# Kernel optimization log

Measured on AMD Instinct MI355X. Metric: run time of the kernel, lower is better.

Reference implementation:

```python
import jax, jax.numpy as jnp
import numpy as np

B, T, I, H, O = 64, 512, 256, 1024, 256


def setup_inputs() -> dict:
    key = jax.random.key(0)
    ks = jax.random.split(key, 12)
    s_i = 1.0 / np.sqrt(H)
    u = lambda k, shape: jax.random.uniform(k, shape, jnp.float32, -s_i, s_i)
    return {
        "x": jax.random.normal(ks[0], (B, T, I), jnp.float32),
        "enc_Wih": u(ks[1], (4 * H, I)),
        "enc_Whh": u(ks[2], (4 * H, H)),
        "enc_bih": u(ks[3], (4 * H,)),
        "enc_bhh": u(ks[4], (4 * H,)),
        "dec_Wih": u(ks[5], (4 * H, I)),
        "dec_Whh": u(ks[6], (4 * H, H)),
        "dec_bih": u(ks[7], (4 * H,)),
        "dec_bhh": u(ks[8], (4 * H,)),
        "fc_W": u(ks[9], (O, H)),
        "fc_b": u(ks[10], (O,)),
    }


def _lstm_gates(pre):
    # torch gate order: i, f, g, o
    i, f, g, o = jnp.split(pre, 4, axis=-1)
    return jax.nn.sigmoid(i), jax.nn.sigmoid(f), jnp.tanh(g), jax.nn.sigmoid(o)


def reference(x, enc_Wih, enc_Whh, enc_bih, enc_bhh,
              dec_Wih, dec_Whh, dec_bih, dec_bhh, fc_W, fc_b):
    # ---- encoder: LSTM scan over time, zero initial state ----
    b = enc_bih + enc_bhh  # [4H]
    # precompute input projections for all steps: [T, B, 4H]
    x_t = jnp.swapaxes(x, 0, 1)  # [T, B, I]
    xproj = jnp.einsum('tbi,gi->tbg', x_t, enc_Wih) + b

    def cell(carry, xp):
        h, c = carry
        pre = xp + h @ enc_Whh.T  # [B, 4H]
        i, f, g, o = _lstm_gates(pre)
        c = f * c + i * g
        h = o * jnp.tanh(c)
        return (h, c), None

    h0 = jnp.zeros((B, H), x.dtype)
    c0 = jnp.zeros((B, H), x.dtype)
    (h, c), _ = jax.lax.scan(cell, (h0, c0), xproj)

    # ---- decoder: each frame is ONE LSTM cell step from the SAME (h, c),
    # since the torch loop re-passes encoder state every iteration -> batch over T.
    pre = (jnp.einsum('bti,gi->btg', x, dec_Wih)
           + (h @ dec_Whh.T + dec_bih + dec_bhh)[:, None, :])  # [B, T, 4H]
    i, f, g, o = _lstm_gates(pre)
    c_new = f * c[:, None, :] + i * g          # [B, T, H]
    h_new = o * jnp.tanh(c_new)                # [B, T, H]
    pred = jnp.einsum('bth,oh->bto', h_new, fc_W) + fc_b  # [B, T, O]
    return pred
```

## Files before the change

### kernel.cpp

```cpp
#include <hip/hip_runtime.h>
#include <hip/hip_bf16.h>

#define BB 64
#define TT_ 512
#define IN_ 256
#define HH 1024
#define G4 4096
#define OO 256

typedef _Float16 half8 __attribute__((ext_vector_type(8)));
typedef float f32x4 __attribute__((ext_vector_type(4)));
typedef unsigned int uint4v __attribute__((ext_vector_type(4)));

__device__ __forceinline__ float sigmoidf_(float v) {
    return 1.f / (1.f + __expf(-v));
}
__device__ __forceinline__ float tanhf_(float v) {
    float vc = fminf(fmaxf(v, -15.f), 15.f);
    float e = __expf(2.f * vc);
    return (e - 1.f) / (e + 1.f);
}

__global__ __launch_bounds__(256)
void pack_a2(const float* __restrict__ Whh, const float* __restrict__ Wih,
             _Float16* __restrict__ Apk)
{
    int id = blockIdx.x * 256 + threadIdx.x;
    int dq  = id / 5120;
    int r1  = id - dq * 5120;
    int t2  = r1 / 2560;
    int r2  = r1 - t2 * 2560;
    int kc  = r2 >> 6, l = r2 & 63;
    int rD  = l & 15;
    int g   = rD & 3, ddl = rD >> 2;
    int d   = dq * 8 + t2 * 4 + ddl;
    int j   = g * HH + d;
    int k0  = kc * 32 + ((l >> 4) << 3);
    half8 v;
    if (kc < 32) {
        const float* s = Whh + (size_t)j * HH + k0;
#pragma unroll
        for (int e = 0; e < 8; ++e) v[e] = (_Float16)s[e];
    } else {
        const float* s = Wih + (size_t)j * IN_ + (k0 - 1024);
#pragma unroll
        for (int e = 0; e < 8; ++e) v[e] = (_Float16)s[e];
    }
    ((half8*)Apk)[id] = v;
}

__global__ __launch_bounds__(256)
void pack_ahh(const float* __restrict__ Whh, _Float16* __restrict__ Ahhpk)
{
    int id = blockIdx.x * 256 + threadIdx.x;
    int jt = id >> 11;
    int r  = id & 2047;
    int kc = r >> 6, l = r & 63;
    int rD = l & 15, g = rD & 3, ddl = rD >> 2;
    int d  = jt * 4 + ddl;
    int j  = g * HH + d;
    int k0 = kc * 32 + ((l >> 4) << 3);
    const float* s = Whh + (size_t)j * HH + k0;
    half8 v;
#pragma unroll
    for (int e = 0; e < 8; ++e) v[e] = (_Float16)s[e];
    ((half8*)Ahhpk)[id] = v;
}

__global__ __launch_bounds__(256)
void pack_adec(const float* __restrict__ Wih, _Float16* __restrict__ Adecpk)
{
    int id = blockIdx.x * 256 + threadIdx.x;
    int dq = id >> 10;
    int r1 = id & 1023;
    int t2 = r1 >> 9;
    int r2 = r1 & 511;
    int kc2 = r2 >> 6, l = r2 & 63;
    int rD = l & 15, g = rD & 3, ddl = rD >> 2;
    int d  = dq * 8 + t2 * 4 + ddl;
    int j  = g * HH + d;
    int k0 = kc2 * 32 + ((l >> 4) << 3);
    const float* s = Wih + (size_t)j * IN_ + k0;
    half8 v;
#pragma unroll
    for (int e = 0; e < 8; ++e) v[e] = (_Float16)s[e];
    ((half8*)Adecpk)[id] = v;
}

__global__ __launch_bounds__(256)
void pack_fcw(const float* __restrict__ fcW, _Float16* __restrict__ fcWpk)
{
    int id = blockIdx.x * 256 + threadIdx.x;
    int ot = id >> 11;
    int r  = id & 2047;
    int kc = r >> 6, l = r & 63;
    int o  = ot * 16 + (l & 15);
    int k0 = kc * 32 + ((l >> 4) << 3);
    const float* s = fcW + (size_t)o * HH + k0;
    half8 v;
#pragma unroll
    for (int e = 0; e < 8; ++e) v[e] = (_Float16)s[e];
    ((half8*)fcWpk)[id] = v;
}

__global__ __launch_bounds__(256)
void pack_x(const float* __restrict__ x, _Float16* __restrict__ Xpk)
{
    int id = blockIdx.x * 256 + threadIdx.x;
    int l = id & 63, bt = (id >> 6) & 3, kc2 = (id >> 8) & 7, t = id >> 11;
    int b  = bt * 16 + (l & 15);
    int i0 = kc2 * 32 + ((l >> 4) << 3);
    const float* s = x + ((size_t)b * TT_ + t) * IN_ + i0;
    half8 v;
#pragma unroll
    for (int e = 0; e < 8; ++e) v[e] = (_Float16)s[e];
    ((half8*)Xpk)[id] = v;
}

__global__ __launch_bounds__(256)
void pack_bias(const float* __restrict__ bih, const float* __restrict__ bhh,
               float* __restrict__ biasc)
{
    int j = blockIdx.x * 256 + threadIdx.x;
    if (j < G4) biasc[j] = bih[j] + bhh[j];
}

__global__ __launch_bounds__(256, 1)
void enc_persist(const _Float16* __restrict__ Apk,
                 const _Float16* __restrict__ Xpk,
                 _Float16* __restrict__ Hbuf,
                 const float* __restrict__ biasc,
                 float* __restrict__ cT)
{
    __shared__ __align__(16) _Float16 Ald[4 * 32 * 64 * 8];
    __shared__ __align__(16) f32x4 pp[16 * 64];
    const int tid  = threadIdx.x;
    const int lane = tid & 63, w = tid >> 6;
    const int dq16 = blockIdx.x >> 2, grp = blockIdx.x & 3;
    const int q = lane >> 4, bl = lane & 15;
    const int d = dq16 * 16 + w * 4 + q;
    const int b = grp * 16 + bl;

    {
        const half8* src = (const half8*)Apk + ((size_t)(dq16 * 4 + w) * 40) * 64 + lane;
        half8* dst = (half8*)Ald + (size_t)w * 2048 + lane;
#pragma unroll
        for (int kc = 0; kc < 32; ++kc) dst[kc * 64] = src[kc * 64];
    }
    half8 xa[8];
    {
        const half8* src = (const half8*)Apk + ((size_t)(dq16 * 4 + w) * 40 + 32) * 64 + lane;
#pragma unroll
        for (int k = 0; k < 8; ++k) xa[k] = src[k * 64];
    }

    float bsum[4];
#pragma unroll
    for (int g = 0; g < 4; ++g) bsum[g] = biasc[g * HH + d];

    const half8* Ald8 = (const half8*)Ald + lane;

    const unsigned int pidx = ((unsigned)grp * 2048 + ((unsigned)d >> 5) * 64 +
                               (((unsigned)d >> 3) & 3) * 16 + bl) * 8 + (d & 7);

    float c_reg = 0.f;
    __syncthreads();

    for (int t = 0; t < TT_; ++t) {
        const int sIn  = (t - 1) & 63;
        const int sOut = t & 63;
        const int sPoi = (t + 8) & 63;

        const uint4v* Xsrc = (const uint4v*)Xpk + ((size_t)t * 32 + grp) * 64 + lane;
        uint4v xft[8];
#pragma unroll
        for (int k = 0; k < 8; ++k) {
            asm volatile("global_load_dwordx4 %0, %1, off"
                         : "=v"(xft[k]) : "v"(Xsrc + k * 256));
        }
        uint4v tmp[8];
        const uint4v* Hsrc = (const uint4v*)Hbuf + (size_t)sIn * 8192 +
                             (size_t)grp * 2048;
        if (t > 0) {
#pragma unroll
            for (int i = 0; i < 8; ++i) {
                asm volatile("global_load_dwordx4 %0, %1, off sc0 sc1"
                             : "=v"(tmp[i]) : "v"(Hsrc + i * 256 + tid));
            }
            asm volatile("s_waitcnt vmcnt(8)" ::: "memory");
        } else {
            asm volatile("s_waitcnt vmcnt(0)" ::: "memory");
        }
        __builtin_amdgcn_sched_barrier(0);

        f32x4 accX = {0.f, 0.f, 0.f, 0.f};
#pragma unroll
        for (int k = 0; k < 8; ++k) {
            half8 bf = __builtin_bit_cast(half8, xft[k]);
            accX = __builtin_amdgcn_mfma_f32_16x16x32_f16(xa[k], bf, accX, 0, 0, 0);
        }

        f32x4 accT[4];
#pragma unroll
        for (int jl = 0; jl < 4; ++jl) accT[jl] = (f32x4){0.f, 0.f, 0.f, 0.f};

        if (t > 0) {
            for (;;) {
                asm volatile("s_waitcnt vmcnt(0)" ::: "memory");
                __builtin_amdgcn_sched_barrier(0);
                int bad[8];
                int any = 0;
#pragma unroll
                for (int i = 0; i < 8; ++i) {
                    bad[i] = (tmp[i].x == 0xFFFFFFFFu) | (tmp[i].y == 0xFFFFFFFFu) |
                             (tmp[i].z == 0xFFFFFFFFu) | (tmp[i].w == 0xFFFFFFFFu);
                    any |= bad[i];
                }
                if (__all(any == 0)) break;
#pragma unroll
                for (int i = 0; i < 8; ++i) {
                    if (bad[i]) {
                        asm volatile("global_load_dwordx4 %0, %1, off sc0 sc1"
                                     : "=v"(tmp[i]) : "v"(Hsrc + i * 256 + tid));
                    }
                }
                __builtin_amdgcn_s_sleep(1);
            }

#pragma unroll
            for (int i = 0; i < 8; ++i) {
                const int kc = i * 4 + w;
                half8 bf = __builtin_bit_cast(half8, tmp[i]);
#pragma unroll
                for (int jl = 0; jl < 4; ++jl) {
                    half8 a = Ald8[jl * 2048 + kc * 64];
                    accT[jl] = __builtin_amdgcn_mfma_f32_16x16x32_f16(a, bf, accT[jl], 0, 0, 0);
                }
            }
        }

#pragma unroll
        for (int jl = 0; jl < 4; ++jl)
            pp[(w * 4 + jl) * 64 + lane] = accT[jl];
        __syncthreads();

        f32x4 s = accX;
#pragma unroll
        for (int w2 = 0; w2 < 4; ++w2)
            s += pp[(w2 * 4 + w) * 64 + lane];

        float pi = s[0] + bsum[0];
        float pf = s[1] + bsum[1];
        float pg = s[2] + bsum[2];
        float po = s[3] + bsum[3];
        float ig = sigmoidf_(pi), fg = sigmoidf_(pf);
        float gg = tanhf_(pg),    og = sigmoidf_(po);
        c_reg = fg * c_reg + ig * gg;
        float h = og * tanhf_(c_reg);

        float hp = __shfl_xor(h, 16);
        if (!(q & 1)) {
            _Float16 h0 = (_Float16)h, h1 = (_Float16)hp;
            unsigned int pk = (unsigned int)__builtin_bit_cast(unsigned short, h0) |
                              ((unsigned int)__builtin_bit_cast(unsigned short, h1) << 16);
            unsigned int* po_ = (unsigned int*)(Hbuf + (size_t)sOut * 65536 + pidx);
            asm volatile("global_store_dword %0, %1, off sc0 sc1"
                         :: "v"(po_), "v"(pk) : "memory");
            unsigned int* pz = (unsigned int*)(Hbuf + (size_t)sPoi * 65536 + pidx);
            unsigned int poison = 0xFFFFFFFFu;
            asm volatile("global_store_dword %0, %1, off sc0 sc1"
                         :: "v"(pz), "v"(poison) : "memory");
        }

        if (t < TT_ - 1) __syncthreads();
    }

    cT[d * 64 + b] = c_reg;
}

__global__ __launch_bounds__(256)
void hdec_mfma(const _Float16* __restrict__ Ahhpk,
               const _Float16* __restrict__ Hfin,
               const float* __restrict__ biascd,
               float* __restrict__ hdecg)
{
    const int tid = threadIdx.x;
    const int lane = tid & 63, w = tid >> 6;
    const int jt = blockIdx.x * 4 + w;
    const int q = lane >> 4, bl = lane & 15;

    const half8* A8 = (const half8*)Ahhpk + ((size_t)jt * 32) * 64 + lane;
    const half8* H8 = (const half8*)Hfin + lane;

    f32x4 acc[4];
#pragma unroll
    for (int g = 0; g < 4; ++g) acc[g] = (f32x4){0.f, 0.f, 0.f, 0.f};
#pragma unroll 4
    for (int kc = 0; kc < 32; ++kc) {
        half8 a = A8[kc * 64];
#pragma unroll
        for (int g = 0; g < 4; ++g) {
            half8 bf = H8[g * 2048 + kc * 64];
            acc[g] = __builtin_amdgcn_mfma_f32_16x16x32_f16(a, bf, acc[g], 0, 0, 0);
        }
    }
    int d = jt * 4 + q;
#pragma unroll
    for (int g = 0; g < 4; ++g)
#pragma unroll
        for (int r = 0; r < 4; ++r)
            hdecg[((size_t)r * HH + d) * 64 + g * 16 + bl] = acc[g][r] + biascd[r * HH + d];
}

__global__ __launch_bounds__(256)
void dec_mfma(const _Float16* __restrict__ Adecpk,
              const _Float16* __restrict__ fcWpk,
              const _Float16* __restrict__ Xpk,
              const float* __restrict__ hdecg,
              const float* __restrict__ cT,
              const float* __restrict__ fcb,
              float* __restrict__ out)
{
    __shared__ __align__(16) _Float16 Hn[32 * 64 * 8];
    __shared__ __align__(16) float outl[16][260];
    const int tid = threadIdx.x;
    const int lane = tid & 63, w = tid >> 6;
    const int t = blockIdx.x >> 2, bq4 = blockIdx.x & 3;
    const int q = lane >> 4, bl = lane & 15;
    const int bg = bq4 * 16 + bl;

    const half8* X8 = (const half8*)Xpk + ((size_t)t * 32 + bq4) * 64 + lane;
    half8 xf[8];
#pragma unroll
    for (int kc2 = 0; kc2 < 8; ++kc2) xf[kc2] = X8[kc2 * 256];

    const half8* AD = (const half8*)Adecpk + lane;
    for (int dqi = 0; dqi < 32; ++dqi) {
        int dq = w * 32 + dqi;
#pragma unroll
        for (int t2 = 0; t2 < 2; ++t2) {
            f32x4 acc = {0.f, 0.f, 0.f, 0.f};
#pragma unroll
            for (int kc2 = 0; kc2 < 8; ++kc2) {
                half8 a = AD[((size_t)(dq * 2 + t2) * 8 + kc2) * 64];
                acc = __builtin_amdgcn_mfma_f32_16x16x32_f16(a, xf[kc2], acc, 0, 0, 0);
            }
            int d = dq * 8 + t2 * 4 + q;
            float cv = cT[d * 64 + bg];
            float pi = acc[0] + hdecg[(size_t)(0 * HH + d) * 64 + bg];
            float pf = acc[1] + hdecg[(size_t)(1 * HH + d) * 64 + bg];
            float pg = acc[2] + hdecg[(size_t)(2 * HH + d) * 64 + bg];
            float po = acc[3] + hdecg[(size_t)(3 * HH + d) * 64 + bg];
            float ig = sigmoidf_(pi), fg = sigmoidf_(pf);
            float gg = tanhf_(pg),    og = sigmoidf_(po);
            float cn = fg * cv + ig * gg;
            float h = og * tanhf_(cn);
            Hn[((d >> 5) * 64 + ((d >> 3) & 3) * 16 + bl) * 8 + (d & 7)] = (_Float16)h;
        }
    }
    __syncthreads();

    const half8* Hn8 = (const half8*)Hn + lane;
    const half8* FW = (const half8*)fcWpk + lane;
#pragma unroll
    for (int oti = 0; oti < 4; ++oti) {
        int ot = w * 4 + oti;
        f32x4 acc = {0.f, 0.f, 0.f, 0.f};
        for (int kc = 0; kc < 32; ++kc) {
            half8 a  = FW[((size_t)ot * 32 + kc) * 64];
            half8 bf = Hn8[kc * 64];
            acc = __builtin_amdgcn_mfma_f32_16x16x32_f16(a, bf, acc, 0, 0, 0);
        }
#pragma unroll
        for (int r = 0; r < 4; ++r) {
            int o = ot * 16 + q * 4 + r;
            outl[bl][o] = acc[r] + fcb[o];
        }
    }
    __syncthreads();

#pragma unroll
    for (int i = 0; i < 16; ++i) {
        int b = bq4 * 16 + i;
        out[((size_t)b * TT_ + t) * OO + tid] = outl[i][tid];
    }
}

extern "C" void kernel_launch(void* const* d_in, const int* in_sizes, int n_in,
                              void* d_out, int out_size, void* d_ws, size_t ws_size,
                              hipStream_t stream) {
    const float* x    = (const float*)d_in[0];
    const float* eWih = (const float*)d_in[1];
    const float* eWhh = (const float*)d_in[2];
    const float* ebih = (const float*)d_in[3];
    const float* ebhh = (const float*)d_in[4];
    const float* dWih = (const float*)d_in[5];
    const float* dWhh = (const float*)d_in[6];
    const float* dbih = (const float*)d_in[7];
    const float* dbhh = (const float*)d_in[8];
    const float* fcW  = (const float*)d_in[9];
    const float* fcb  = (const float*)d_in[10];

    float* ws     = (float*)d_ws;
    float* cT     = ws;
    float* hdecg  = ws + 65536;
    float* biasc  = ws + 327680;
    float* biascd = ws + 331776;
    _Float16* fp  = (_Float16*)(ws + 335872);
    _Float16* Hbuf = fp;
    _Float16* Apk  = fp + 4194304;
    _Float16* Xpk  = Apk + 5242880;
    _Float16* Adecpk = Xpk + 8388608;
    _Float16* fcWpk  = Adecpk + 1048576;
    _Float16* Ahhpk  = fcWpk + 262144;

    pack_a2<<<dim3(2560), dim3(256), 0, stream>>>(eWhh, eWih, Apk);
    pack_x<<<dim3(4096), dim3(256), 0, stream>>>(x, Xpk);
    pack_bias<<<dim3(16), dim3(256), 0, stream>>>(ebih, ebhh, biasc);
    pack_bias<<<dim3(16), dim3(256), 0, stream>>>(dbih, dbhh, biascd);
    pack_adec<<<dim3(512), dim3(256), 0, stream>>>(dWih, Adecpk);
    pack_fcw<<<dim3(128), dim3(256), 0, stream>>>(fcW, fcWpk);
    pack_ahh<<<dim3(2048), dim3(256), 0, stream>>>(dWhh, Ahhpk);
    hipMemsetAsync(Hbuf, 0xFF, (size_t)4194304 * sizeof(_Float16), stream);

    enc_persist<<<dim3(256), dim3(256), 0, stream>>>(
        Apk, Xpk, Hbuf, biasc, cT);

    const _Float16* Hfin = Hbuf + (size_t)((TT_ - 1) & 63) * 65536;
    hdec_mfma<<<dim3(64), dim3(256), 0, stream>>>(Ahhpk, Hfin, biascd, hdecg);
    dec_mfma<<<dim3(2048), dim3(256), 0, stream>>>(Adecpk, fcWpk, Xpk, hdecg, cT,
                                                   fcb, (float*)d_out);
}
```

Measured before the change: 1.493 ms.

## Fuse pack kernels, double-buffer encoder reduction scratch, process two timesteps per decoder block

All packing kernels and the Hbuf poison memset are merged into one launch to cut launch overhead. The encoder double-buffers its cross-wave partial-sum shared array, which lets it drop one of the two block barriers per timestep. The decoder handles two timesteps per block so each weight fragment load feeds two MFMAs, halving decoder weight traffic at the cost of more registers and shared memory. Dropping the barrier relies on the parity buffer preventing races between consecutive steps.

```diff
diff --git a/kernel.cpp b/kernel.cpp
--- a/kernel.cpp
+++ b/kernel.cpp
@@ -22,107 +22,106 @@
 }
 
 __global__ __launch_bounds__(256)
-void pack_a2(const float* __restrict__ Whh, const float* __restrict__ Wih,
-             _Float16* __restrict__ Apk)
+void pack_all(const float* __restrict__ eWhh, const float* __restrict__ eWih,
+              const float* __restrict__ x,
+              const float* __restrict__ ebih, const float* __restrict__ ebhh,
+              const float* __restrict__ dbih, const float* __restrict__ dbhh,
+              const float* __restrict__ dWih, const float* __restrict__ fcW,
+              const float* __restrict__ dWhh,
+              _Float16* __restrict__ Apk, _Float16* __restrict__ Xpk,
+              float* __restrict__ biasc, float* __restrict__ biascd,
+              _Float16* __restrict__ Adecpk, _Float16* __restrict__ fcWpk,
+              _Float16* __restrict__ Ahhpk, _Float16* __restrict__ Hbuf)
 {
-    int id = blockIdx.x * 256 + threadIdx.x;
-    int dq  = id / 5120;
-    int r1  = id - dq * 5120;
-    int t2  = r1 / 2560;
-    int r2  = r1 - t2 * 2560;
-    int kc  = r2 >> 6, l = r2 & 63;
-    int rD  = l & 15;
-    int g   = rD & 3, ddl = rD >> 2;
-    int d   = dq * 8 + t2 * 4 + ddl;
-    int j   = g * HH + d;
-    int k0  = kc * 32 + ((l >> 4) << 3);
-    half8 v;
-    if (kc < 32) {
-        const float* s = Whh + (size_t)j * HH + k0;
+    const int blk = blockIdx.x;
+    if (blk < 2560) {
+        int id = blk * 256 + threadIdx.x;
+        int dq  = id / 5120;
+        int r1  = id - dq * 5120;
+        int t2  = r1 / 2560;
+        int r2  = r1 - t2 * 2560;
+        int kc  = r2 >> 6, l = r2 & 63;
+        int rD  = l & 15;
+        int g   = rD & 3, ddl = rD >> 2;
+        int d   = dq * 8 + t2 * 4 + ddl;
+        int j   = g * HH + d;
+        int k0  = kc * 32 + ((l >> 4) << 3);
+        half8 v;
+        if (kc < 32) {
+            const float* s = eWhh + (size_t)j * HH + k0;
+#pragma unroll
+            for (int e = 0; e < 8; ++e) v[e] = (_Float16)s[e];
+        } else {
+            const float* s = eWih + (size_t)j * IN_ + (k0 - 1024);
+#pragma unroll
+            for (int e = 0; e < 8; ++e) v[e] = (_Float16)s[e];
+        }
+        ((half8*)Apk)[id] = v;
+    } else if (blk < 6656) {
+        int id = (blk - 2560) * 256 + threadIdx.x;
+        int l = id & 63, bt = (id >> 6) & 3, kc2 = (id >> 8) & 7, t = id >> 11;
+        int b  = bt * 16 + (l & 15);
+        int i0 = kc2 * 32 + ((l >> 4) << 3);
+        const float* s = x + ((size_t)b * TT_ + t) * IN_ + i0;
+        half8 v;
 #pragma unroll
         for (int e = 0; e < 8; ++e) v[e] = (_Float16)s[e];
+        ((half8*)Xpk)[id] = v;
+    } else if (blk < 6672) {
+        int j = (blk - 6656) * 256 + threadIdx.x;
+        if (j < G4) biasc[j] = ebih[j] + ebhh[j];
+    } else if (blk < 6688) {
+        int j = (blk - 6672) * 256 + threadIdx.x;
+        if (j < G4) biascd[j] = dbih[j] + dbhh[j];
+    } else if (blk < 7200) {
+        int id = (blk - 6688) * 256 + threadIdx.x;
+        int dq = id >> 10;
+        int r1 = id & 1023;
+        int t2 = r1 >> 9;
+        int r2 = r1 & 511;
+        int kc2 = r2 >> 6, l = r2 & 63;
+        int rD = l & 15, g = rD & 3, ddl = rD >> 2;
+        int d  = dq * 8 + t2 * 4 + ddl;
+        int j  = g * HH + d;
+        int k0 = kc2 * 32 + ((l >> 4) << 3);
+        const float* s = dWih + (size_t)j * IN_ + k0;
+        half8 v;
+#pragma unroll
+        for (int e = 0; e < 8; ++e) v[e] = (_Float16)s[e];
+        ((half8*)Adecpk)[id] = v;
+    } else if (blk < 7328) {
+        int id = (blk - 7200) * 256 + threadIdx.x;
+        int ot = id >> 11;
+        int r  = id & 2047;
+        int kc = r >> 6, l = r & 63;
+        int o  = ot * 16 + (l & 15);
+        int k0 = kc * 32 + ((l >> 4) << 3);
+        const float* s = fcW + (size_t)o * HH + k0;
+        half8 v;
+#pragma unroll
+        for (int e = 0; e < 8; ++e) v[e] = (_Float16)s[e];
+        ((half8*)fcWpk)[id] = v;
+    } else if (blk < 9376) {
+        int id = (blk - 7328) * 256 + threadIdx.x;
+        int jt = id >> 11;
+        int r  = id & 2047;
+        int kc = r >> 6, l = r & 63;
+        int rD = l & 15, g = rD & 3, ddl = rD >> 2;
+        int d  = jt * 4 + ddl;
+        int j  = g * HH + d;
+        int k0 = kc * 32 + ((l >> 4) << 3);
+        const float* s = dWhh + (size_t)j * HH + k0;
+        half8 v;
+#pragma unroll
+        for (int e = 0; e < 8; ++e) v[e] = (_Float16)s[e];
+        ((half8*)Ahhpk)[id] = v;
     } else {
-        const float* s = Wih + (size_t)j * IN_ + (k0 - 1024);
-#pragma unroll
-        for (int e = 0; e < 8; ++e) v[e] = (_Float16)s[e];
-    }
-    ((half8*)Apk)[id] = v;
-}
-
-__global__ __launch_bounds__(256)
-void pack_ahh(const float* __restrict__ Whh, _Float16* __restrict__ Ahhpk)
-{
-    int id = blockIdx.x * 256 + threadIdx.x;
-    int jt = id >> 11;
-    int r  = id & 2047;
-    int kc = r >> 6, l = r & 63;
-    int rD = l & 15, g = rD & 3, ddl = rD >> 2;
-    int d  = jt * 4 + ddl;
-    int j  = g * HH + d;
-    int k0 = kc * 32 + ((l >> 4) << 3);
-    const float* s = Whh + (size_t)j * HH + k0;
-    half8 v;
-#pragma unroll
-    for (int e = 0; e < 8; ++e) v[e] = (_Float16)s[e];
-    ((half8*)Ahhpk)[id] = v;
-}
-
-__global__ __launch_bounds__(256)
-void pack_adec(const float* __restrict__ Wih, _Float16* __restrict__ Adecpk)
-{
-    int id = blockIdx.x * 256 + threadIdx.x;
-    int dq = id >> 10;
-    int r1 = id & 1023;
-    int t2 = r1 >> 9;
-    int r2 = r1 & 511;
-    int kc2 = r2 >> 6, l = r2 & 63;
-    int rD = l & 15, g = rD & 3, ddl = rD >> 2;
-    int d  = dq * 8 + t2 * 4 + ddl;
-    int j  = g * HH + d;
-    int k0 = kc2 * 32 + ((l >> 4) << 3);
-    const float* s = Wih + (size_t)j * IN_ + k0;
-    half8 v;
-#pragma unroll
-    for (int e = 0; e < 8; ++e) v[e] = (_Float16)s[e];
-    ((half8*)Adecpk)[id] = v;
-}
-
-__global__ __launch_bounds__(256)
-void pack_fcw(const float* __restrict__ fcW, _Float16* __restrict__ fcWpk)
-{
-    int id = blockIdx.x * 256 + threadIdx.x;
-    int ot = id >> 11;
-    int r  = id & 2047;
-    int kc = r >> 6, l = r & 63;
-    int o  = ot * 16 + (l & 15);
-    int k0 = kc * 32 + ((l >> 4) << 3);
-    const float* s = fcW + (size_t)o * HH + k0;
-    half8 v;
-#pragma unroll
-    for (int e = 0; e < 8; ++e) v[e] = (_Float16)s[e];
-    ((half8*)fcWpk)[id] = v;
-}
-
-__global__ __launch_bounds__(256)
-void pack_x(const float* __restrict__ x, _Float16* __restrict__ Xpk)
-{
-    int id = blockIdx.x * 256 + threadIdx.x;
-    int l = id & 63, bt = (id >> 6) & 3, kc2 = (id >> 8) & 7, t = id >> 11;
-    int b  = bt * 16 + (l & 15);
-    int i0 = kc2 * 32 + ((l >> 4) << 3);
-    const float* s = x + ((size_t)b * TT_ + t) * IN_ + i0;
-    half8 v;
-#pragma unroll
-    for (int e = 0; e < 8; ++e) v[e] = (_Float16)s[e];
-    ((half8*)Xpk)[id] = v;
-}
-
-__global__ __launch_bounds__(256)
-void pack_bias(const float* __restrict__ bih, const float* __restrict__ bhh,
-               float* __restrict__ biasc)
-{
-    int j = blockIdx.x * 256 + threadIdx.x;
-    if (j < G4) biasc[j] = bih[j] + bhh[j];
+        uint4v* H4 = (uint4v*)Hbuf;
+        int base = (blk - 9376) * 1024 + threadIdx.x;
+        uint4v p = {0xFFFFFFFFu, 0xFFFFFFFFu, 0xFFFFFFFFu, 0xFFFFFFFFu};
+#pragma unroll
+        for (int i = 0; i < 4; ++i) H4[base + i * 256] = p;
+    }
 }
 
 __global__ __launch_bounds__(256, 1)
@@ -133,7 +132,7 @@
                  float* __restrict__ cT)
 {
     __shared__ __align__(16) _Float16 Ald[4 * 32 * 64 * 8];
-    __shared__ __align__(16) f32x4 pp[16 * 64];
+    __shared__ __align__(16) f32x4 pp[2][16 * 64];
     const int tid  = threadIdx.x;
     const int lane = tid & 63, w = tid >> 6;
     const int dq16 = blockIdx.x >> 2, grp = blockIdx.x & 3;
@@ -170,6 +169,7 @@
         const int sIn  = (t - 1) & 63;
         const int sOut = t & 63;
         const int sPoi = (t + 8) & 63;
+        const int pb   = t & 1;
 
         const uint4v* Xsrc = (const uint4v*)Xpk + ((size_t)t * 32 + grp) * 64 + lane;
         uint4v xft[8];
@@ -241,13 +241,13 @@
 
 #pragma unroll
         for (int jl = 0; jl < 4; ++jl)
-            pp[(w * 4 + jl) * 64 + lane] = accT[jl];
+            pp[pb][(w * 4 + jl) * 64 + lane] = accT[jl];
         __syncthreads();
 
         f32x4 s = accX;
 #pragma unroll
         for (int w2 = 0; w2 < 4; ++w2)
-            s += pp[(w2 * 4 + w) * 64 + lane];
+            s += pp[pb][(w2 * 4 + w) * 64 + lane];
 
         float pi = s[0] + bsum[0];
         float pf = s[1] + bsum[1];
@@ -271,8 +271,6 @@
             asm volatile("global_store_dword %0, %1, off sc0 sc1"
                          :: "v"(pz), "v"(poison) : "memory");
         }
-
-        if (t < TT_ - 1) __syncthreads();
     }
 
     cT[d * 64 + b] = c_reg;
@@ -313,76 +311,92 @@
 }
 
 __global__ __launch_bounds__(256)
-void dec_mfma(const _Float16* __restrict__ Adecpk,
-              const _Float16* __restrict__ fcWpk,
-              const _Float16* __restrict__ Xpk,
-              const float* __restrict__ hdecg,
-              const float* __restrict__ cT,
-              const float* __restrict__ fcb,
-              float* __restrict__ out)
+void dec_mfma2(const _Float16* __restrict__ Adecpk,
+               const _Float16* __restrict__ fcWpk,
+               const _Float16* __restrict__ Xpk,
+               const float* __restrict__ hdecg,
+               const float* __restrict__ cT,
+               const float* __restrict__ fcb,
+               float* __restrict__ out)
 {
-    __shared__ __align__(16) _Float16 Hn[32 * 64 * 8];
+    __shared__ __align__(16) _Float16 Hn[2][32 * 64 * 8];
     __shared__ __align__(16) float outl[16][260];
     const int tid = threadIdx.x;
     const int lane = tid & 63, w = tid >> 6;
-    const int t = blockIdx.x >> 2, bq4 = blockIdx.x & 3;
+    const int tp = blockIdx.x >> 2, bq4 = blockIdx.x & 3;
+    const int t0 = tp * 2;
     const int q = lane >> 4, bl = lane & 15;
     const int bg = bq4 * 16 + bl;
 
-    const half8* X8 = (const half8*)Xpk + ((size_t)t * 32 + bq4) * 64 + lane;
-    half8 xf[8];
-#pragma unroll
-    for (int kc2 = 0; kc2 < 8; ++kc2) xf[kc2] = X8[kc2 * 256];
+    const half8* X0 = (const half8*)Xpk + ((size_t)t0 * 32 + bq4) * 64 + lane;
+    const half8* X1 = (const half8*)Xpk + ((size_t)(t0 + 1) * 32 + bq4) * 64 + lane;
+    half8 xf0[8], xf1[8];
+#pragma unroll
+    for (int k = 0; k < 8; ++k) { xf0[k] = X0[k * 256]; xf1[k] = X1[k * 256]; }
 
     const half8* AD = (const half8*)Adecpk + lane;
     for (int dqi = 0; dqi < 32; ++dqi) {
         int dq = w * 32 + dqi;
 #pragma unroll
         for (int t2 = 0; t2 < 2; ++t2) {
-            f32x4 acc = {0.f, 0.f, 0.f, 0.f};
+            f32x4 acc0 = {0.f, 0.f, 0.f, 0.f};
+            f32x4 acc1 = {0.f, 0.f, 0.f, 0.f};
 #pragma unroll
             for (int kc2 = 0; kc2 < 8; ++kc2) {
                 half8 a = AD[((size_t)(dq * 2 + t2) * 8 + kc2) * 64];
-                acc = __builtin_amdgcn_mfma_f32_16x16x32_f16(a, xf[kc2], acc, 0, 0, 0);
+                acc0 = __builtin_amdgcn_mfma_f32_16x16x32_f16(a, xf0[kc2], acc0, 0, 0, 0);
+                acc1 = __builtin_amdgcn_mfma_f32_16x16x32_f16(a, xf1[kc2], acc1, 0, 0, 0);
             }
             int d = dq * 8 + t2 * 4 + q;
             float cv = cT[d * 64 + bg];
-            float pi = acc[0] + hdecg[(size_t)(0 * HH + d) * 64 + bg];
-            float pf = acc[1] + hdecg[(size_t)(1 * HH + d) * 64 + bg];
-            float pg = acc[2] + hdecg[(size_t)(2 * HH + d) * 64 + bg];
-            float po = acc[3] + hdecg[(size_t)(3 * HH + d) * 64 + bg];
-            float ig = sigmoidf_(pi), fg = sigmoidf_(pf);
-            float gg = tanhf_(pg),    og = sigmoidf_(po);
-            float cn = fg * cv + ig * gg;
-            float h = og * tanhf_(cn);
-            Hn[((d >> 5) * 64 + ((d >> 3) & 3) * 16 + bl) * 8 + (d & 7)] = (_Float16)h;
+            float hbi = hdecg[(size_t)(0 * HH + d) * 64 + bg];
+            float hbf = hdecg[(size_t)(1 * HH + d) * 64 + bg];
+            float hbg = hdecg[(size_t)(2 * HH + d) * 64 + bg];
+            float hbo = hdecg[(size_t)(3 * HH + d) * 64 + bg];
+            unsigned int hidx = (((unsigned)d >> 5) * 64 +
+                                 (((unsigned)d >> 3) & 3) * 16 + bl) * 8 + (d & 7);
+            {
+                float ig = sigmoidf_(acc0[0] + hbi), fg = sigmoidf_(acc0[1] + hbf);
+                float gg = tanhf_(acc0[2] + hbg),    og = sigmoidf_(acc0[3] + hbo);
+                float cn = fg * cv + ig * gg;
+                Hn[0][hidx] = (_Float16)(og * tanhf_(cn));
+            }
+            {
+                float ig = sigmoidf_(acc1[0] + hbi), fg = sigmoidf_(acc1[1] + hbf);
+                float gg = tanhf_(acc1[2] + hbg),    og = sigmoidf_(acc1[3] + hbo);
+                float cn = fg * cv + ig * gg;
+                Hn[1][hidx] = (_Float16)(og * tanhf_(cn));
+            }
         }
     }
     __syncthreads();
 
-    const half8* Hn8 = (const half8*)Hn + lane;
     const half8* FW = (const half8*)fcWpk + lane;
 #pragma unroll
-    for (int oti = 0; oti < 4; ++oti) {
-        int ot = w * 4 + oti;
-        f32x4 acc = {0.f, 0.f, 0.f, 0.f};
-        for (int kc = 0; kc < 32; ++kc) {
-            half8 a  = FW[((size_t)ot * 32 + kc) * 64];
-            half8 bf = Hn8[kc * 64];
-            acc = __builtin_amdgcn_mfma_f32_16x16x32_f16(a, bf, acc, 0, 0, 0);
-        }
-#pragma unroll
-        for (int r = 0; r < 4; ++r) {
-            int o = ot * 16 + q * 4 + r;
-            outl[bl][o] = acc[r] + fcb[o];
-        }
-    }
-    __syncthreads();
-
-#pragma unroll
-    for (int i = 0; i < 16; ++i) {
-        int b = bq4 * 16 + i;
-        out[((size_t)b * TT_ + t) * OO + tid] = outl[i][tid];
+    for (int tt = 0; tt < 2; ++tt) {
+        const half8* Hn8 = (const half8*)&Hn[tt][0] + lane;
+#pragma unroll
+        for (int oti = 0; oti < 4; ++oti) {
+            int ot = w * 4 + oti;
+            f32x4 acc = {0.f, 0.f, 0.f, 0.f};
+            for (int kc = 0; kc < 32; ++kc) {
+                half8 a  = FW[((size_t)ot * 32 + kc) * 64];
+                half8 bf = Hn8[kc * 64];
+                acc = __builtin_amdgcn_mfma_f32_16x16x32_f16(a, bf, acc, 0, 0, 0);
+            }
+#pragma unroll
+            for (int r = 0; r < 4; ++r) {
+                int o = ot * 16 + q * 4 + r;
+                outl[bl][o] = acc[r] + fcb[o];
+            }
+        }
+        __syncthreads();
+#pragma unroll
+        for (int i = 0; i < 16; ++i) {
+            int b = bq4 * 16 + i;
+            out[((size_t)b * TT_ + t0 + tt) * OO + tid] = outl[i][tid];
+        }
+        __syncthreads();
     }
 }
 
@@ -414,20 +428,15 @@
     _Float16* fcWpk  = Adecpk + 1048576;
     _Float16* Ahhpk  = fcWpk + 262144;
 
-    pack_a2<<<dim3(2560), dim3(256), 0, stream>>>(eWhh, eWih, Apk);
-    pack_x<<<dim3(4096), dim3(256), 0, stream>>>(x, Xpk);
-    pack_bias<<<dim3(16), dim3(256), 0, stream>>>(ebih, ebhh, biasc);
-    pack_bias<<<dim3(16), dim3(256), 0, stream>>>(dbih, dbhh, biascd);
-    pack_adec<<<dim3(512), dim3(256), 0, stream>>>(dWih, Adecpk);
-    pack_fcw<<<dim3(128), dim3(256), 0, stream>>>(fcW, fcWpk);
-    pack_ahh<<<dim3(2048), dim3(256), 0, stream>>>(dWhh, Ahhpk);
-    hipMemsetAsync(Hbuf, 0xFF, (size_t)4194304 * sizeof(_Float16), stream);
+    pack_all<<<dim3(9888), dim3(256), 0, stream>>>(
+        eWhh, eWih, x, ebih, ebhh, dbih, dbhh, dWih, fcW, dWhh,
+        Apk, Xpk, biasc, biascd, Adecpk, fcWpk, Ahhpk, Hbuf);
 
     enc_persist<<<dim3(256), dim3(256), 0, stream>>>(
         Apk, Xpk, Hbuf, biasc, cT);
 
     const _Float16* Hfin = Hbuf + (size_t)((TT_ - 1) & 63) * 65536;
     hdec_mfma<<<dim3(64), dim3(256), 0, stream>>>(Ahhpk, Hfin, biascd, hdecg);
-    dec_mfma<<<dim3(2048), dim3(256), 0, stream>>>(Adecpk, fcWpk, Xpk, hdecg, cT,
-                                                   fcb, (float*)d_out);
-}
+    dec_mfma2<<<dim3(1024), dim3(256), 0, stream>>>(Adecpk, fcWpk, Xpk, hdecg, cT,
+                                                    fcb, (float*)d_out);
+}
```

Measured after the change: 1.755 ms. 17.5% more time.
